# Kernel optimization log

Measured on AMD Instinct MI355X. Metric: run time of the kernel, lower is better.

The kernel has to match this reference:

```python
import jax, jax.numpy as jnp
import numpy as np

N = 50000
E = 800000
DIN = 64
DOUT = 64
H = 4
C = DOUT // H
EPS = 1e-5


def setup_inputs() -> dict:
    key = jax.random.key(0)
    ks = jax.random.split(key, 40)
    inp = {}
    inp["x"] = jax.random.normal(ks[0], (N, DIN), jnp.float32)
    inp["edge_index"] = jax.random.randint(ks[1], (2, E), 0, N, dtype=jnp.int32)
    inp["edge_weight"] = jax.random.uniform(ks[2], (E,), jnp.float32)
    inp["edge_attr"] = jax.random.normal(ks[3], (E, 1), jnp.float32)
    k = 4
    for i in range(2):
        din = DIN if i == 0 else DOUT
        s = din ** -0.5
        inp[f"gcn_w{i}"] = jax.random.normal(ks[k], (din, DOUT), jnp.float32) * s; k += 1
        inp[f"gcn_b{i}"] = jnp.zeros((DOUT,), jnp.float32)
        inp[f"res_w{i}"] = jax.random.normal(ks[k], (din, DOUT), jnp.float32) * s; k += 1
        inp[f"res_b{i}"] = jnp.zeros((DOUT,), jnp.float32)
        inp[f"ln_g{i}"] = jnp.ones((DOUT,), jnp.float32)
        inp[f"ln_b{i}"] = jnp.zeros((DOUT,), jnp.float32)
        sg = DOUT ** -0.5
        inp[f"gat_w{i}"] = jax.random.normal(ks[k], (DOUT, H * C), jnp.float32) * sg; k += 1
        inp[f"gat_b{i}"] = jnp.zeros((H * C,), jnp.float32)
        inp[f"att_src{i}"] = jax.random.normal(ks[k], (H, C), jnp.float32) * (C ** -0.5); k += 1
        inp[f"att_dst{i}"] = jax.random.normal(ks[k], (H, C), jnp.float32) * (C ** -0.5); k += 1
        inp[f"att_e{i}"] = jax.random.normal(ks[k], (H, C), jnp.float32) * (C ** -0.5); k += 1
        inp[f"ew_w{i}"] = jax.random.normal(ks[k], (1, H * C), jnp.float32); k += 1
    return inp


def _gcn(x, src0, dst0, ew, W, b):
    n = x.shape[0]
    sl = jnp.arange(n, dtype=src0.dtype)
    src = jnp.concatenate([src0, sl])
    dst = jnp.concatenate([dst0, sl])
    w = jnp.concatenate([ew, jnp.ones((n,), ew.dtype)])  # self-loop weight 1
    deg = jax.ops.segment_sum(w, dst, num_segments=n)
    dinv = jnp.where(deg > 0, jax.lax.rsqrt(deg), 0.0)
    norm = dinv[src] * w * dinv[dst]
    h = x @ W  # [n, DOUT]
    out = jax.ops.segment_sum(h[src] * norm[:, None], dst, num_segments=n)
    return out + b


def _gat(x, src0, dst0, ea, W, b, a_src, a_dst, a_e, We):
    n = x.shape[0]
    sl = jnp.arange(n, dtype=src0.dtype)
    src = jnp.concatenate([src0, sl])
    dst = jnp.concatenate([dst0, sl])
    loop_attr = jnp.broadcast_to(ea.mean(axis=0, keepdims=True), (n, ea.shape[1]))
    ea2 = jnp.concatenate([ea, loop_attr], axis=0)  # fill_value='mean'
    xl = (x @ W).reshape(n, H, C)
    a_s = (xl * a_src).sum(-1)  # [n,H]
    a_d = (xl * a_dst).sum(-1)
    a_ee = ((ea2 @ We).reshape(-1, H, C) * a_e).sum(-1)  # [E2,H]
    alpha = jax.nn.leaky_relu(a_s[src] + a_d[dst] + a_ee, 0.2)
    m = jax.ops.segment_max(alpha, dst, num_segments=n)
    e = jnp.exp(alpha - m[dst])
    s = jax.ops.segment_sum(e, dst, num_segments=n)
    alpha = e / (s[dst] + 1e-16)
    out = jax.ops.segment_sum(xl[src] * alpha[:, :, None], dst, num_segments=n)
    return out.reshape(n, H * C) + b


def _ln(x, g, b):
    mu = x.mean(-1, keepdims=True)
    v = ((x - mu) ** 2).mean(-1, keepdims=True)
    return (x - mu) * jax.lax.rsqrt(v + EPS) * g + b


def reference(x, edge_index, edge_weight, edge_attr,
              gcn_w0, gcn_b0, res_w0, res_b0, ln_g0, ln_b0,
              gat_w0, gat_b0, att_src0, att_dst0, att_e0, ew_w0,
              gcn_w1, gcn_b1, res_w1, res_b1, ln_g1, ln_b1,
              gat_w1, gat_b1, att_src1, att_dst1, att_e1, ew_w1):
    src0, dst0 = edge_index[0], edge_index[1]
    layers = [
        (gcn_w0, gcn_b0, res_w0, res_b0, ln_g0, ln_b0, gat_w0, gat_b0, att_src0, att_dst0, att_e0, ew_w0),
        (gcn_w1, gcn_b1, res_w1, res_b1, ln_g1, ln_b1, gat_w1, gat_b1, att_src1, att_dst1, att_e1, ew_w1),
    ]
    for (gw, gb, rw, rb, lg, lb, Wg, bg, a_s, a_d, a_e, We) in layers:
        residual = x @ rw + rb
        x = jax.nn.silu(_gcn(x, src0, dst0, edge_weight, gw, gb)) + residual
        x = _ln(x, lg, lb)
        x = jax.nn.silu(_gat(x, src0, dst0, edge_attr, Wg, bg, a_s, a_d, a_e, We)) + x
    return x  # down_sample=False -> Identity
```

## Files before the change

kernel.cpp:

```cpp
#include <hip/hip_runtime.h>
#include <hip/hip_fp16.h>

#define NN 50000
#define NE 800000
#define D 64
#define EPS 1e-5f
#define NT 3125
#define NB1 250
#define EPB 3200
#define NBIN 196
#define STOT 49152
#define SBLK 192

typedef unsigned short ushort_t;
typedef unsigned int uint_t;
typedef __attribute__((ext_vector_type(8))) short bf16x8;
typedef __attribute__((ext_vector_type(4))) float f32x4;

__device__ __forceinline__ float wave_sum64(float v) {
#pragma unroll
  for (int m = 1; m <= 32; m <<= 1) v += __shfl_xor(v, m, 64);
  return v;
}
__device__ __forceinline__ int wave_sum64i(int v) {
#pragma unroll
  for (int m = 1; m <= 32; m <<= 1) v += __shfl_xor(v, m, 64);
  return v;
}
__device__ __forceinline__ float group_sum16(float v) {
#pragma unroll
  for (int m = 1; m <= 8; m <<= 1) v += __shfl_xor(v, m, 64);
  return v;
}
__device__ __forceinline__ float silu_f(float v) { return v / (1.f + __expf(-v)); }
__device__ __forceinline__ float lrelu_f(float v) { return v >= 0.f ? v : 0.2f * v; }
__device__ __forceinline__ ushort_t f2b(float x) {
  unsigned u = __float_as_uint(x);
  return (ushort_t)((u + 0x7FFFu + ((u >> 16) & 1u)) >> 16);
}
__device__ __forceinline__ float b2f(ushort_t u) {
  return __uint_as_float(((unsigned)u) << 16);
}
__device__ __forceinline__ ushort_t f2h(float x) {
  return __half_as_ushort(__float2half_rn(x));
}
__device__ __forceinline__ float h2f(unsigned u) {
  return __half2float(__ushort_as_half((ushort_t)(u & 0xFFFFu)));
}
__device__ __forceinline__ float sel4(float a, float b, float c, float d, int h) {
  float ab = (h & 1) ? b : a;
  float cd = (h & 1) ? d : c;
  return (h & 2) ? cd : ab;
}
__device__ __forceinline__ bf16x8 pack8(float4 a, float4 b) {
  bf16x8 r;
  r[0] = (short)f2b(a.x); r[1] = (short)f2b(a.y);
  r[2] = (short)f2b(a.z); r[3] = (short)f2b(a.w);
  r[4] = (short)f2b(b.x); r[5] = (short)f2b(b.y);
  r[6] = (short)f2b(b.z); r[7] = (short)f2b(b.w);
  return r;
}

__global__ void __launch_bounds__(256) k_pre(
    const int* __restrict__ ei, int* __restrict__ histG,
    const float* __restrict__ x, const float* __restrict__ W1,
    const float* __restrict__ W2, const float* __restrict__ b2,
    ushort_t* __restrict__ out1, float* __restrict__ out2) {
  __shared__ __align__(16) char smem[16384];
  if (blockIdx.x < NB1) {
    int* h = (int*)smem;
    int blk = blockIdx.x;
    for (int j = threadIdx.x; j < NBIN; j += 256) h[j] = 0;
    __syncthreads();
    int e0 = blk * EPB;
    for (int e = e0 + threadIdx.x; e < e0 + EPB; e += 256)
      atomicAdd(&h[ei[NE + e] >> 8], 1);
    __syncthreads();
    for (int j = threadIdx.x; j < NBIN; j += 256) histG[j * NB1 + blk] = h[j];
    return;
  }
  ushort_t* wf = (ushort_t*)smem;
  for (int e = threadIdx.x; e < 8192; e += 256) {
    int f = e >> 9, r = e & 511;
    int lane = r >> 3, j = r & 7;
    int m = f >> 3, s = (f >> 2) & 1, t = f & 3;
    int k = s * 32 + (lane >> 4) * 8 + j;
    int n = t * 16 + (lane & 15);
    const float* Wm = m ? W2 : W1;
    wf[e] = f2b(Wm[k * D + n]);
  }
  __syncthreads();
  int tile = (blockIdx.x - NB1) * 4 + (threadIdx.x >> 6);
  if (tile >= NT) return;
  int l = threadIdx.x & 63;
  int q = l >> 4, cn = l & 15;
  const float* xr = x + ((size_t)tile * 16 + cn) * D + q * 8;
  float4 xa = *(const float4*)xr;
  float4 xb = *(const float4*)(xr + 4);
  float4 xc = *(const float4*)(xr + 32);
  float4 xd = *(const float4*)(xr + 36);
  bf16x8 a0 = pack8(xa, xb), a1 = pack8(xc, xd);
  f32x4 acc1[4], acc2[4];
#pragma unroll
  for (int t = 0; t < 4; ++t) {
    bf16x8 b10 = *(const bf16x8*)&wf[(0 * 8 + 0 * 4 + t) * 512 + l * 8];
    bf16x8 b11 = *(const bf16x8*)&wf[(0 * 8 + 1 * 4 + t) * 512 + l * 8];
    bf16x8 b20 = *(const bf16x8*)&wf[(1 * 8 + 0 * 4 + t) * 512 + l * 8];
    bf16x8 b21 = *(const bf16x8*)&wf[(1 * 8 + 1 * 4 + t) * 512 + l * 8];
    f32x4 z = {0.f, 0.f, 0.f, 0.f};
    acc1[t] = __builtin_amdgcn_mfma_f32_16x16x32_bf16(a0, b10, z, 0, 0, 0);
    acc1[t] = __builtin_amdgcn_mfma_f32_16x16x32_bf16(a1, b11, acc1[t], 0, 0, 0);
    acc2[t] = __builtin_amdgcn_mfma_f32_16x16x32_bf16(a0, b20, z, 0, 0, 0);
    acc2[t] = __builtin_amdgcn_mfma_f32_16x16x32_bf16(a1, b21, acc2[t], 0, 0, 0);
  }
#pragma unroll
  for (int t = 0; t < 4; ++t) {
    float bb = b2[t * 16 + cn];
#pragma unroll
    for (int r = 0; r < 4; ++r) {
      size_t row = (size_t)tile * 16 + q * 4 + r;
      out1[row * D + t * 16 + cn] = f2b(acc1[t][r]);
      out2[row * D + t * 16 + cn] = acc2[t][r] + bb;
    }
  }
}

__global__ void __launch_bounds__(256) k_scanA(
    int* __restrict__ histG, int* __restrict__ bsum, float* __restrict__ scal,
    const float* __restrict__ Wg0, const float* __restrict__ Wg1,
    const float* __restrict__ W11, const float* __restrict__ W21,
    const float* __restrict__ We0, const float* __restrict__ ae0,
    const float* __restrict__ We1, const float* __restrict__ ae1,
    ushort_t* __restrict__ wg16, ushort_t* __restrict__ wd16,
    float* __restrict__ wea2) {
  if (blockIdx.x == SBLK) {
    int tid = threadIdx.x;
    for (int t = tid; t < 1024; t += 256) scal[t] = 0.f;
    for (int e = tid; e < 4096; e += 256) {
      int f = e >> 9, r = e & 511;
      int lane = r >> 3, j = r & 7;
      int s = (f >> 2) & 1, t = f & 3;
      int k = s * 32 + (lane >> 4) * 8 + j;
      int n = t * 16 + (lane & 15);
      wg16[e] = f2b(Wg0[k * D + n]);
      wg16[4096 + e] = f2b(Wg1[k * D + n]);
    }
    for (int e = tid; e < 8192; e += 256) {
      int f = e >> 9, r = e & 511;
      int lane = r >> 3, j = r & 7;
      int m = f >> 3, s = (f >> 2) & 1, t = f & 3;
      int k = s * 32 + (lane >> 4) * 8 + j;
      int n = t * 16 + (lane & 15);
      const float* Wm = m ? W21 : W11;
      wd16[e] = f2b(Wm[k * D + n]);
    }
    if (tid < 64) {
      float v = group_sum16(We0[tid] * ae0[tid]);
      if ((tid & 15) == 0) wea2[tid >> 4] = v;
    } else if (tid < 128) {
      int c = tid - 64;
      float v = group_sum16(We1[c] * ae1[c]);
      if ((c & 15) == 0) wea2[4 + (c >> 4)] = v;
    }
    return;
  }
  __shared__ int sm[256];
  int j = threadIdx.x;
  int i = blockIdx.x * 256 + j;
  const int TOT = NBIN * NB1;
  int v = (i < TOT) ? histG[i] : 0;
  sm[j] = v;
  __syncthreads();
  for (int off = 1; off < 256; off <<= 1) {
    int t = (j >= off) ? sm[j - off] : 0;
    __syncthreads();
    sm[j] += t;
    __syncthreads();
  }
  if (i < TOT) histG[i] = sm[j] - v;
  if (j == 255) bsum[blockIdx.x] = sm[255];
}

__global__ void __launch_bounds__(256) k_scanC(int* __restrict__ histG,
                                               const int* __restrict__ bsum) {
  __shared__ int ws4[4];
  int t = threadIdx.x;
  int v = (t < (int)blockIdx.x) ? bsum[t] : 0;
  v = wave_sum64i(v);
  if ((t & 63) == 0) ws4[t >> 6] = v;
  __syncthreads();
  int prefix = ws4[0] + ws4[1] + ws4[2] + ws4[3];
  int i = blockIdx.x * 256 + t;
  if (i < NBIN * NB1) histG[i] += prefix;
}

__global__ void __launch_bounds__(256) k_part(
    const int* __restrict__ ei, const float* __restrict__ ew,
    const float* __restrict__ ea, const int* __restrict__ histG,
    uint2* __restrict__ rectmp, float* __restrict__ scal) {
  __shared__ int cur[NBIN];
  int blk = blockIdx.x;
  for (int j = threadIdx.x; j < NBIN; j += 256) cur[j] = histG[j * NB1 + blk];
  __syncthreads();
  int e0 = blk * EPB;
  float asum = 0.f;
  for (int e = e0 + threadIdx.x; e < e0 + EPB; e += 256) {
    int src = ei[e];
    int dst = ei[NE + e];
    float w = ew[e];
    float a = ea[e];
    asum += a;
    int slot = atomicAdd(&cur[dst >> 8], 1);
    uint2 r;
    r.x = (uint_t)(src & 0xFFFF) | ((uint_t)f2h(w) << 16);
    r.y = (uint_t)(dst & 0xFF) | ((uint_t)f2h(a) << 16);
    rectmp[slot] = r;
  }
  float s = wave_sum64(asum);
  if ((threadIdx.x & 63) == 0) {
    int slot = (blk * 4 + (threadIdx.x >> 6)) & 63;
    atomicAdd(&scal[(size_t)slot * 16], s);
  }
}

__global__ void __launch_bounds__(256) k_sfin(
    const uint2* __restrict__ rectmp, const int* __restrict__ histG,
    uint_t* __restrict__ recw, uint_t* __restrict__ reca, int* __restrict__ rs,
    float* __restrict__ dinv, float* __restrict__ scal) {
  __shared__ int cnt[256], sc[256], cur[256];
  __shared__ float wsum[256];
  int b = blockIdx.x;
  int t = threadIdx.x;
  int lo = histG[b * NB1];
  int hi = (b == NBIN - 1) ? NE : histG[(b + 1) * NB1];
  cnt[t] = 0;
  wsum[t] = 0.f;
  __syncthreads();
  for (int e = lo + t; e < hi; e += 256)
    atomicAdd(&cnt[rectmp[e].y & 0xFFu], 1);
  __syncthreads();
  int v = cnt[t];
  sc[t] = v;
  __syncthreads();
  for (int off = 1; off < 256; off <<= 1) {
    int u = (t >= off) ? sc[t - off] : 0;
    __syncthreads();
    sc[t] += u;
    __syncthreads();
  }
  int ex = sc[t] - v;
  int node = b * 256 + t;
  if (node < NN) rs[node] = lo + ex;
  if (b == NBIN - 1 && t == 0) rs[NN] = NE;
  cur[t] = lo + ex;
  __syncthreads();
  for (int e = lo + t; e < hi; e += 256) {
    uint2 r = rectmp[e];
    int dl = (int)(r.y & 0xFFu);
    int slot = atomicAdd(&cur[dl], 1);
    atomicAdd(&wsum[dl], h2f(r.x >> 16));
    uint_t src = r.x & 0xFFFFu;
    recw[slot] = r.x;
    reca[slot] = src | (r.y & 0xFFFF0000u);
  }
  __syncthreads();
  if (node < NN) dinv[node] = rsqrtf(1.f + wsum[t]);
  if (b == 0 && t == 0) {
    float s = 0.f;
    for (int j = 0; j < 64; ++j) s += scal[(size_t)j * 16];
    scal[1] = s / (float)NE;
  }
}

__global__ void __launch_bounds__(256) k_gcn_gat(
    const ushort_t* __restrict__ h16, const float* __restrict__ res,
    const float* __restrict__ dinv, const int* __restrict__ rs,
    const uint_t* __restrict__ recw,
    const float* __restrict__ gb, const float* __restrict__ lg,
    const float* __restrict__ lb,
    const ushort_t* __restrict__ wg, const float* __restrict__ att_src,
    const float* __restrict__ att_dst,
    float* __restrict__ x2, ushort_t* __restrict__ xl,
    float* __restrict__ a_s, float* __restrict__ a_d) {
  __shared__ int ss[4][64];
  __shared__ float swt[4][64];
  __shared__ __align__(16) ushort_t xt[16][72];
  int w = threadIdx.x >> 6;
  int l = threadIdx.x & 63;
  int base = blockIdx.x * 8;
  int iA = base + 2 * w;
  int iB = iA + 1;
  int half = l >> 5, cp = l & 31;
  float diA = dinv[iA], diB = dinv[iB];
  float accA = diA * diA * b2f(h16[(size_t)iA * D + l]);
  float accB = diB * diB * b2f(h16[(size_t)iB * D + l]);
  int kA = rs[iA], kA1 = rs[iA + 1];
  int kB = rs[iB], kB1 = rs[iB + 1];
  while (kA < kA1 || kB < kB1) {
    int cntA = min(32, kA1 - kA);
    int cntB = min(32, kB1 - kB);
    int src = 0; float wn = 0.f;
    if (half == 0) {
      if (cp < cntA) {
        uint_t r = recw[(size_t)(kA + cp)];
        src = (int)(r & 0xFFFFu);
        wn = dinv[src] * h2f(r >> 16) * diA;
      }
    } else {
      if (cp < cntB) {
        uint_t r = recw[(size_t)(kB + cp)];
        src = (int)(r & 0xFFFFu);
        wn = dinv[src] * h2f(r >> 16) * diB;
      }
    }
    ss[w][l] = src;
    swt[w][l] = wn;
    int nm = max(cntA, cntB);
    int j = 0;
    for (; j + 4 <= nm; j += 4) {
      int4 sa = *(const int4*)&ss[w][j];
      int4 sb = *(const int4*)&ss[w][32 + j];
      float4 wa = *(const float4*)&swt[w][j];
      float4 wb = *(const float4*)&swt[w][32 + j];
      float a0 = b2f(h16[(size_t)sa.x * D + l]);
      float b0 = b2f(h16[(size_t)sb.x * D + l]);
      float a1 = b2f(h16[(size_t)sa.y * D + l]);
      float b1 = b2f(h16[(size_t)sb.y * D + l]);
      float a2 = b2f(h16[(size_t)sa.z * D + l]);
      float b2v = b2f(h16[(size_t)sb.z * D + l]);
      float a3 = b2f(h16[(size_t)sa.w * D + l]);
      float b3 = b2f(h16[(size_t)sb.w * D + l]);
      accA = fmaf(wa.x, a0, accA); accB = fmaf(wb.x, b0, accB);
      accA = fmaf(wa.y, a1, accA); accB = fmaf(wb.y, b1, accB);
      accA = fmaf(wa.z, a2, accA); accB = fmaf(wb.z, b2v, accB);
      accA = fmaf(wa.w, a3, accA); accB = fmaf(wb.w, b3, accB);
    }
    for (; j < nm; ++j) {
      int sA = ss[w][j], sB = ss[w][32 + j];
      float wA = swt[w][j], wB = swt[w][32 + j];
      float vA = b2f(h16[(size_t)sA * D + l]);
      float vB = b2f(h16[(size_t)sB * D + l]);
      accA = fmaf(wA, vA, accA);
      accB = fmaf(wB, vB, accB);
    }
    kA += cntA; kB += cntB;
  }
  float gbv = gb[l], lgv = lg[l], lbv = lb[l];
  float x1A = silu_f(accA + gbv) + res[(size_t)iA * D + l];
  float x1B = silu_f(accB + gbv) + res[(size_t)iB * D + l];
  float muA = wave_sum64(x1A) * (1.f / 64.f);
  float muB = wave_sum64(x1B) * (1.f / 64.f);
  float dA = x1A - muA, dB = x1B - muB;
  float varA = wave_sum64(dA * dA) * (1.f / 64.f);
  float varB = wave_sum64(dB * dB) * (1.f / 64.f);
  float oA = dA * rsqrtf(varA + EPS) * lgv + lbv;
  float oB = dB * rsqrtf(varB + EPS) * lgv + lbv;
  x2[(size_t)iA * D + l] = oA;
  x2[(size_t)iB * D + l] = oB;
  xt[2 * w][l] = f2b(oA);
  xt[2 * w + 1][l] = f2b(oB);
  {
    ushort_t* xz = &xt[8][0];
    for (int e = threadIdx.x; e < 8 * 72; e += 256) xz[e] = 0;
  }
  __syncthreads();
  int t = w;
  int q = l >> 4, cn = l & 15;
  bf16x8 a0 = *(const bf16x8*)&xt[cn][q * 8];
  bf16x8 a1 = *(const bf16x8*)&xt[cn][q * 8 + 32];
  bf16x8 b0 = *(const bf16x8*)&wg[(size_t)((0 * 4 + t) * 512 + l * 8)];
  bf16x8 b1 = *(const bf16x8*)&wg[(size_t)((1 * 4 + t) * 512 + l * 8)];
  f32x4 z = {0.f, 0.f, 0.f, 0.f};
  f32x4 acc = __builtin_amdgcn_mfma_f32_16x16x32_bf16(a0, b0, z, 0, 0, 0);
  acc = __builtin_amdgcn_mfma_f32_16x16x32_bf16(a1, b1, acc, 0, 0, 0);
  if (q < 2) {
    float av = att_src[t * 16 + cn];
    float dv = att_dst[t * 16 + cn];
#pragma unroll
    for (int r = 0; r < 4; ++r) {
      size_t row = (size_t)base + q * 4 + r;
      xl[row * D + t * 16 + cn] = f2b(acc[r]);
      float vs = group_sum16(acc[r] * av);
      float vd = group_sum16(acc[r] * dv);
      if (cn == 0) {
        a_s[row * 4 + t] = vs;
        a_d[row * 4 + t] = vd;
      }
    }
  }
}

template <int FUSE>
__global__ void __launch_bounds__(256) k_gat_fin(
    const ushort_t* __restrict__ xl16, const float* __restrict__ x2,
    const float* __restrict__ a_s, const float* __restrict__ a_d,
    const int* __restrict__ rs, const uint_t* __restrict__ reca,
    const float* __restrict__ wea, const float* __restrict__ scal,
    const float* __restrict__ bg,
    const ushort_t* __restrict__ wd, const float* __restrict__ b2,
    ushort_t* __restrict__ out1, float* __restrict__ out2,
    float* __restrict__ xout) {
  __shared__ int ss[4][64];
  __shared__ float el[4][4][68];
  __shared__ __align__(16) ushort_t xt[16][72];
  int w = threadIdx.x >> 6;
  int base = blockIdx.x * 8;
  int iA = base + 2 * w;
  int iB = iA + 1;
  int l = threadIdx.x & 63;
  int half = l >> 5, cp = l & 31;
  int hh = l >> 4;
  float4 wv4 = *(const float4*)wea;
  float mean_attr = scal[1];
  float we_h = sel4(wv4.x, wv4.y, wv4.z, wv4.w, hh);
  float ad_hA = a_d[(size_t)iA * 4 + hh], as_iA = a_s[(size_t)iA * 4 + hh];
  float ad_hB = a_d[(size_t)iB * 4 + hh], as_iB = a_s[(size_t)iB * 4 + hh];
  float eSA = __expf(lrelu_f(as_iA + ad_hA + mean_attr * we_h));
  float eSB = __expf(lrelu_f(as_iB + ad_hB + mean_attr * we_h));
  float sA = eSA, sB = eSB;
  float accA = eSA * b2f(xl16[(size_t)iA * D + l]);
  float accB = eSB * b2f(xl16[(size_t)iB * D + l]);
  const float* adp = a_d + (size_t)(half ? iB : iA) * 4;
  float4 ad4 = *(const float4*)adp;
  int kA = rs[iA], kA1 = rs[iA + 1];
  int kB = rs[iB], kB1 = rs[iB + 1];
  while (kA < kA1 || kB < kB1) {
    int cntA = min(32, kA1 - kA);
    int cntB = min(32, kB1 - kB);
    int myk = half ? kB : kA;
    int mycnt = half ? cntB : cntA;
    int src = 0;
    float e0v = 0.f, e1v = 0.f, e2v = 0.f, e3v = 0.f;
    if (cp < mycnt) {
      uint_t r = reca[(size_t)(myk + cp)];
      src = (int)(r & 0xFFFFu);
      float ea = h2f(r >> 16);
      float4 as4 = *(const float4*)(a_s + (size_t)src * 4);
      e0v = __expf(lrelu_f(as4.x + fmaf(ea, wv4.x, ad4.x)));
      e1v = __expf(lrelu_f(as4.y + fmaf(ea, wv4.y, ad4.y)));
      e2v = __expf(lrelu_f(as4.z + fmaf(ea, wv4.z, ad4.z)));
      e3v = __expf(lrelu_f(as4.w + fmaf(ea, wv4.w, ad4.w)));
    }
    ss[w][l] = src;
    el[w][0][l] = e0v;
    el[w][1][l] = e1v;
    el[w][2][l] = e2v;
    el[w][3][l] = e3v;
    int nm = max(cntA, cntB);
    int j = 0;
    for (; j + 4 <= nm; j += 4) {
      int4 sa = *(const int4*)&ss[w][j];
      int4 sb = *(const int4*)&ss[w][32 + j];
      float4 ea4 = *(const float4*)&el[w][hh][j];
      float4 eb4 = *(const float4*)&el[w][hh][32 + j];
      float a0 = b2f(xl16[(size_t)sa.x * D + l]);
      float b0 = b2f(xl16[(size_t)sb.x * D + l]);
      float a1 = b2f(xl16[(size_t)sa.y * D + l]);
      float b1 = b2f(xl16[(size_t)sb.y * D + l]);
      float a2 = b2f(xl16[(size_t)sa.z * D + l]);
      float b2v = b2f(xl16[(size_t)sb.z * D + l]);
      float a3 = b2f(xl16[(size_t)sa.w * D + l]);
      float b3 = b2f(xl16[(size_t)sb.w * D + l]);
      accA = fmaf(ea4.x, a0, accA); accB = fmaf(eb4.x, b0, accB);
      accA = fmaf(ea4.y, a1, accA); accB = fmaf(eb4.y, b1, accB);
      accA = fmaf(ea4.z, a2, accA); accB = fmaf(eb4.z, b2v, accB);
      accA = fmaf(ea4.w, a3, accA); accB = fmaf(eb4.w, b3, accB);
      sA += (ea4.x + ea4.y) + (ea4.z + ea4.w);
      sB += (eb4.x + eb4.y) + (eb4.z + eb4.w);
    }
    for (; j < nm; ++j) {
      int srcA = ss[w][j], srcB = ss[w][32 + j];
      float eA = el[w][hh][j], eB = el[w][hh][32 + j];
      float vA = b2f(xl16[(size_t)srcA * D + l]);
      float vB = b2f(xl16[(size_t)srcB * D + l]);
      accA = fmaf(eA, vA, accA);
      accB = fmaf(eB, vB, accB);
      sA += eA; sB += eB;
    }
    kA += cntA; kB += cntB;
  }
  float bgv = bg[l];
  float oA = accA / (sA + 1e-16f) + bgv;
  float oB = accB / (sB + 1e-16f) + bgv;
  float vA = silu_f(oA) + x2[(size_t)iA * D + l];
  float vB = silu_f(oB) + x2[(size_t)iB * D + l];
  if (FUSE) {
    xt[2 * w][l] = f2b(vA);
    xt[2 * w + 1][l] = f2b(vB);
    {
      ushort_t* xz = &xt[8][0];
      for (int e = threadIdx.x; e < 8 * 72; e += 256) xz[e] = 0;
    }
    __syncthreads();
    int t = w;
    int q = l >> 4, cn = l & 15;
    bf16x8 a0 = *(const bf16x8*)&xt[cn][q * 8];
    bf16x8 a1 = *(const bf16x8*)&xt[cn][q * 8 + 32];
#pragma unroll
    for (int m = 0; m < 2; ++m) {
      bf16x8 b0 = *(const bf16x8*)&wd[(size_t)((m * 8 + 0 * 4 + t) * 512 + l * 8)];
      bf16x8 b1 = *(const bf16x8*)&wd[(size_t)((m * 8 + 1 * 4 + t) * 512 + l * 8)];
      f32x4 z = {0.f, 0.f, 0.f, 0.f};
      f32x4 acc = __builtin_amdgcn_mfma_f32_16x16x32_bf16(a0, b0, z, 0, 0, 0);
      acc = __builtin_amdgcn_mfma_f32_16x16x32_bf16(a1, b1, acc, 0, 0, 0);
      if (q < 2) {
        float bb = (m == 1) ? b2[t * 16 + cn] : 0.f;
#pragma unroll
        for (int r = 0; r < 4; ++r) {
          size_t row = (size_t)base + q * 4 + r;
          if (m == 0)
            out1[row * D + t * 16 + cn] = f2b(acc[r]);
          else
            out2[row * D + t * 16 + cn] = acc[r] + bb;
        }
      }
    }
  } else {
    xout[(size_t)iA * D + l] = vA;
    xout[(size_t)iB * D + l] = vB;
  }
}


extern "C" void kernel_launch(void* const* d_in, const int* in_sizes, int n_in,
                              void* d_out, int out_size, void* d_ws, size_t ws_size,
                              hipStream_t stream) {
  (void)in_sizes; (void)n_in; (void)out_size; (void)ws_size;
  const float* x  = (const float*)d_in[0];
  const int*   ei = (const int*)d_in[1];
  const float* ew = (const float*)d_in[2];
  const float* ea = (const float*)d_in[3];
  const float* P[2][12];
  for (int l = 0; l < 2; ++l)
    for (int j = 0; j < 12; ++j) P[l][j] = (const float*)d_in[4 + l * 12 + j];

  float* W = (float*)d_ws;
  const size_t o_rs    = 0;
  const size_t o_dinv  = o_rs + NN + 16;
  const size_t o_wea   = o_dinv + NN;
  const size_t o_scal  = o_wea + 16;
  const size_t o_bsum  = o_scal + 1024;
  const size_t o_hist  = o_bsum + 256;
  const size_t o_recw  = o_hist + STOT;
  const size_t o_reca  = o_recw + NE;
  const size_t o_rtmp  = o_reca + NE;
  const size_t o_h16   = o_rtmp + (size_t)NE * 2;
  const size_t o_xl16  = o_h16 + (size_t)NN * D / 2;
  const size_t o_res   = o_xl16 + (size_t)NN * D / 2;
  const size_t o_x2    = o_res + (size_t)NN * D;
  const size_t o_as    = o_x2 + (size_t)NN * D;
  const size_t o_ad    = o_as + (size_t)NN * 4;
  const size_t o_wg16  = o_ad + (size_t)NN * 4;
  const size_t o_wd16  = o_wg16 + 4096;

  int*      rs    = (int*)(W + o_rs);
  float*    dinv  = W + o_dinv;
  float*    wea2  = W + o_wea;
  float*    scal  = W + o_scal;
  int*      bsum  = (int*)(W + o_bsum);
  int*      histG = (int*)(W + o_hist);
  uint_t*   recw  = (uint_t*)(W + o_recw);
  uint_t*   reca  = (uint_t*)(W + o_reca);
  uint2*    rtmp  = (uint2*)(W + o_rtmp);
  ushort_t* h16   = (ushort_t*)(W + o_h16);
  ushort_t* xl16  = (ushort_t*)(W + o_xl16);
  float*    resb  = W + o_res;
  float*    x2b   = W + o_x2;
  float*    asb   = W + o_as;
  float*    adb   = W + o_ad;
  ushort_t* wg16  = (ushort_t*)(W + o_wg16);
  ushort_t* wd16  = (ushort_t*)(W + o_wd16);

  const int B = 256;
  const int gPre = NB1 + (NT + 3) / 4;
  const int gN2  = NN / 8;

  k_pre<<<gPre, B, 0, stream>>>(ei, histG, x, P[0][0], P[0][2], P[0][3], h16, resb);
  k_scanA<<<SBLK + 1, B, 0, stream>>>(histG, bsum, scal,
                                      P[0][6], P[1][6], P[1][0], P[1][2],
                                      P[0][11], P[0][10], P[1][11], P[1][10],
                                      wg16, wd16, wea2);
  k_scanC<<<SBLK, B, 0, stream>>>(histG, bsum);
  k_part<<<NB1, B, 0, stream>>>(ei, ew, ea, histG, rtmp, scal);
  k_sfin<<<NBIN, B, 0, stream>>>(rtmp, histG, recw, reca, rs, dinv, scal);

  k_gcn_gat<<<gN2, B, 0, stream>>>(h16, resb, dinv, rs, recw,
                                   P[0][1], P[0][4], P[0][5],
                                   wg16, P[0][8], P[0][9],
                                   x2b, xl16, asb, adb);
  k_gat_fin<1><<<gN2, B, 0, stream>>>(xl16, x2b, asb, adb, rs, reca,
                                      wea2, scal, P[0][7],
                                      wd16, P[1][3], h16, resb, nullptr);
  k_gcn_gat<<<gN2, B, 0, stream>>>(h16, resb, dinv, rs, recw,
                                   P[1][1], P[1][4], P[1][5],
                                   wg16 + 4096, P[1][8], P[1][9],
                                   x2b, xl16, asb, adb);
  k_gat_fin<0><<<gN2, B, 0, stream>>>(xl16, x2b, asb, adb, rs, reca,
                                      wea2 + 4, scal, P[1][7],
                                      nullptr, nullptr, nullptr, nullptr,
                                      (float*)d_out);
}
```

Baseline: 293.7 us.

## Remap gather lanes so each half-wave handles one node with 2 features per lane

In the GCN and GAT aggregation kernels, each wave used to process two nodes with every lane gathering one bf16 feature for both nodes. Now each 32-lane half-wave owns one node and each lane loads a packed 32-bit pair of bf16 features per neighbor. This halves the number of gather load instructions and issues wider loads, with per-node reductions done over 32 lanes. The cost is that the loop still runs to the max of the two nodes' degrees, so the half with fewer neighbors idles.

```diff
diff --git a/kernel.cpp b/kernel.cpp
--- a/kernel.cpp
+++ b/kernel.cpp
@@ -22,6 +22,11 @@
   for (int m = 1; m <= 32; m <<= 1) v += __shfl_xor(v, m, 64);
   return v;
 }
+__device__ __forceinline__ float half_sum32(float v) {
+#pragma unroll
+  for (int m = 1; m <= 16; m <<= 1) v += __shfl_xor(v, m, 64);
+  return v;
+}
 __device__ __forceinline__ int wave_sum64i(int v) {
 #pragma unroll
   for (int m = 1; m <= 32; m <<= 1) v += __shfl_xor(v, m, 64);
@@ -40,6 +45,12 @@
 }
 __device__ __forceinline__ float b2f(ushort_t u) {
   return __uint_as_float(((unsigned)u) << 16);
+}
+__device__ __forceinline__ float b2f_lo(uint_t u) {
+  return __uint_as_float(u << 16);
+}
+__device__ __forceinline__ float b2f_hi(uint_t u) {
+  return __uint_as_float(u & 0xFFFF0000u);
 }
 __device__ __forceinline__ ushort_t f2h(float x) {
   return __half_as_ushort(__float2half_rn(x));
@@ -288,77 +299,70 @@
   int w = threadIdx.x >> 6;
   int l = threadIdx.x & 63;
   int base = blockIdx.x * 8;
+  int half = l >> 5, c = l & 31;
   int iA = base + 2 * w;
   int iB = iA + 1;
-  int half = l >> 5, cp = l & 31;
-  float diA = dinv[iA], diB = dinv[iB];
-  float accA = diA * diA * b2f(h16[(size_t)iA * D + l]);
-  float accB = diB * diB * b2f(h16[(size_t)iB * D + l]);
+  int i = iA + half;
+  float di = dinv[i];
+  uint_t u0 = *(const uint_t*)&h16[(size_t)i * D + 2 * c];
+  float dii = di * di;
+  float acc0 = dii * b2f_lo(u0);
+  float acc1 = dii * b2f_hi(u0);
   int kA = rs[iA], kA1 = rs[iA + 1];
   int kB = rs[iB], kB1 = rs[iB + 1];
+  int sbase = half * 32;
   while (kA < kA1 || kB < kB1) {
     int cntA = min(32, kA1 - kA);
     int cntB = min(32, kB1 - kB);
+    int myk = half ? kB : kA;
+    int mycnt = half ? cntB : cntA;
     int src = 0; float wn = 0.f;
-    if (half == 0) {
-      if (cp < cntA) {
-        uint_t r = recw[(size_t)(kA + cp)];
-        src = (int)(r & 0xFFFFu);
-        wn = dinv[src] * h2f(r >> 16) * diA;
-      }
-    } else {
-      if (cp < cntB) {
-        uint_t r = recw[(size_t)(kB + cp)];
-        src = (int)(r & 0xFFFFu);
-        wn = dinv[src] * h2f(r >> 16) * diB;
-      }
+    if (c < mycnt) {
+      uint_t r = recw[(size_t)(myk + c)];
+      src = (int)(r & 0xFFFFu);
+      wn = dinv[src] * h2f(r >> 16) * di;
     }
     ss[w][l] = src;
     swt[w][l] = wn;
     int nm = max(cntA, cntB);
     int j = 0;
     for (; j + 4 <= nm; j += 4) {
-      int4 sa = *(const int4*)&ss[w][j];
-      int4 sb = *(const int4*)&ss[w][32 + j];
-      float4 wa = *(const float4*)&swt[w][j];
-      float4 wb = *(const float4*)&swt[w][32 + j];
-      float a0 = b2f(h16[(size_t)sa.x * D + l]);
-      float b0 = b2f(h16[(size_t)sb.x * D + l]);
-      float a1 = b2f(h16[(size_t)sa.y * D + l]);
-      float b1 = b2f(h16[(size_t)sb.y * D + l]);
-      float a2 = b2f(h16[(size_t)sa.z * D + l]);
-      float b2v = b2f(h16[(size_t)sb.z * D + l]);
-      float a3 = b2f(h16[(size_t)sa.w * D + l]);
-      float b3 = b2f(h16[(size_t)sb.w * D + l]);
-      accA = fmaf(wa.x, a0, accA); accB = fmaf(wb.x, b0, accB);
-      accA = fmaf(wa.y, a1, accA); accB = fmaf(wb.y, b1, accB);
-      accA = fmaf(wa.z, a2, accA); accB = fmaf(wb.z, b2v, accB);
-      accA = fmaf(wa.w, a3, accA); accB = fmaf(wb.w, b3, accB);
+      int4 s4 = *(const int4*)&ss[w][sbase + j];
+      float4 w4 = *(const float4*)&swt[w][sbase + j];
+      uint_t ua = *(const uint_t*)&h16[(size_t)s4.x * D + 2 * c];
+      uint_t ub = *(const uint_t*)&h16[(size_t)s4.y * D + 2 * c];
+      uint_t uc = *(const uint_t*)&h16[(size_t)s4.z * D + 2 * c];
+      uint_t ud = *(const uint_t*)&h16[(size_t)s4.w * D + 2 * c];
+      acc0 = fmaf(w4.x, b2f_lo(ua), acc0); acc1 = fmaf(w4.x, b2f_hi(ua), acc1);
+      acc0 = fmaf(w4.y, b2f_lo(ub), acc0); acc1 = fmaf(w4.y, b2f_hi(ub), acc1);
+      acc0 = fmaf(w4.z, b2f_lo(uc), acc0); acc1 = fmaf(w4.z, b2f_hi(uc), acc1);
+      acc0 = fmaf(w4.w, b2f_lo(ud), acc0); acc1 = fmaf(w4.w, b2f_hi(ud), acc1);
     }
     for (; j < nm; ++j) {
-      int sA = ss[w][j], sB = ss[w][32 + j];
-      float wA = swt[w][j], wB = swt[w][32 + j];
-      float vA = b2f(h16[(size_t)sA * D + l]);
-      float vB = b2f(h16[(size_t)sB * D + l]);
-      accA = fmaf(wA, vA, accA);
-      accB = fmaf(wB, vB, accB);
+      int s1 = ss[w][sbase + j];
+      float w1 = swt[w][sbase + j];
+      uint_t u = *(const uint_t*)&h16[(size_t)s1 * D + 2 * c];
+      acc0 = fmaf(w1, b2f_lo(u), acc0);
+      acc1 = fmaf(w1, b2f_hi(u), acc1);
     }
     kA += cntA; kB += cntB;
   }
-  float gbv = gb[l], lgv = lg[l], lbv = lb[l];
-  float x1A = silu_f(accA + gbv) + res[(size_t)iA * D + l];
-  float x1B = silu_f(accB + gbv) + res[(size_t)iB * D + l];
-  float muA = wave_sum64(x1A) * (1.f / 64.f);
-  float muB = wave_sum64(x1B) * (1.f / 64.f);
-  float dA = x1A - muA, dB = x1B - muB;
-  float varA = wave_sum64(dA * dA) * (1.f / 64.f);
-  float varB = wave_sum64(dB * dB) * (1.f / 64.f);
-  float oA = dA * rsqrtf(varA + EPS) * lgv + lbv;
-  float oB = dB * rsqrtf(varB + EPS) * lgv + lbv;
-  x2[(size_t)iA * D + l] = oA;
-  x2[(size_t)iB * D + l] = oB;
-  xt[2 * w][l] = f2b(oA);
-  xt[2 * w + 1][l] = f2b(oB);
+  float2 gb2 = *(const float2*)&gb[2 * c];
+  float2 lg2 = *(const float2*)&lg[2 * c];
+  float2 lb2 = *(const float2*)&lb[2 * c];
+  float2 rs2 = *(const float2*)&res[(size_t)i * D + 2 * c];
+  float x0 = silu_f(acc0 + gb2.x) + rs2.x;
+  float x1 = silu_f(acc1 + gb2.y) + rs2.y;
+  float mu = half_sum32(x0 + x1) * (1.f / 64.f);
+  float d0 = x0 - mu, d1 = x1 - mu;
+  float var = half_sum32(d0 * d0 + d1 * d1) * (1.f / 64.f);
+  float rinv = rsqrtf(var + EPS);
+  float o0 = d0 * rinv * lg2.x + lb2.x;
+  float o1 = d1 * rinv * lg2.y + lb2.y;
+  float2 o2; o2.x = o0; o2.y = o1;
+  *(float2*)&x2[(size_t)i * D + 2 * c] = o2;
+  uint_t pk = (uint_t)f2b(o0) | ((uint_t)f2b(o1) << 16);
+  *(uint_t*)&xt[2 * w + half][2 * c] = pk;
   {
     ushort_t* xz = &xt[8][0];
     for (int e = threadIdx.x; e < 8 * 72; e += 256) xz[e] = 0;
@@ -404,26 +408,27 @@
   __shared__ float el[4][4][68];
   __shared__ __align__(16) ushort_t xt[16][72];
   int w = threadIdx.x >> 6;
+  int l = threadIdx.x & 63;
   int base = blockIdx.x * 8;
+  int half = l >> 5, c = l & 31;
   int iA = base + 2 * w;
   int iB = iA + 1;
-  int l = threadIdx.x & 63;
-  int half = l >> 5, cp = l & 31;
-  int hh = l >> 4;
+  int i = iA + half;
+  int hh = c >> 3;
   float4 wv4 = *(const float4*)wea;
   float mean_attr = scal[1];
   float we_h = sel4(wv4.x, wv4.y, wv4.z, wv4.w, hh);
-  float ad_hA = a_d[(size_t)iA * 4 + hh], as_iA = a_s[(size_t)iA * 4 + hh];
-  float ad_hB = a_d[(size_t)iB * 4 + hh], as_iB = a_s[(size_t)iB * 4 + hh];
-  float eSA = __expf(lrelu_f(as_iA + ad_hA + mean_attr * we_h));
-  float eSB = __expf(lrelu_f(as_iB + ad_hB + mean_attr * we_h));
-  float sA = eSA, sB = eSB;
-  float accA = eSA * b2f(xl16[(size_t)iA * D + l]);
-  float accB = eSB * b2f(xl16[(size_t)iB * D + l]);
-  const float* adp = a_d + (size_t)(half ? iB : iA) * 4;
-  float4 ad4 = *(const float4*)adp;
+  float ad_h = a_d[(size_t)i * 4 + hh];
+  float as_i = a_s[(size_t)i * 4 + hh];
+  float eS = __expf(lrelu_f(as_i + ad_h + mean_attr * we_h));
+  float s = eS;
+  uint_t u0 = *(const uint_t*)&xl16[(size_t)i * D + 2 * c];
+  float acc0 = eS * b2f_lo(u0);
+  float acc1 = eS * b2f_hi(u0);
+  float4 ad4 = *(const float4*)(a_d + (size_t)i * 4);
   int kA = rs[iA], kA1 = rs[iA + 1];
   int kB = rs[iB], kB1 = rs[iB + 1];
+  int sbase = half * 32;
   while (kA < kA1 || kB < kB1) {
     int cntA = min(32, kA1 - kA);
     int cntB = min(32, kB1 - kB);
@@ -431,8 +436,8 @@
     int mycnt = half ? cntB : cntA;
     int src = 0;
     float e0v = 0.f, e1v = 0.f, e2v = 0.f, e3v = 0.f;
-    if (cp < mycnt) {
-      uint_t r = reca[(size_t)(myk + cp)];
+    if (c < mycnt) {
+      uint_t r = reca[(size_t)(myk + c)];
       src = (int)(r & 0xFFFFu);
       float ea = h2f(r >> 16);
       float4 as4 = *(const float4*)(a_s + (size_t)src * 4);
@@ -449,44 +454,38 @@
     int nm = max(cntA, cntB);
     int j = 0;
     for (; j + 4 <= nm; j += 4) {
-      int4 sa = *(const int4*)&ss[w][j];
-      int4 sb = *(const int4*)&ss[w][32 + j];
-      float4 ea4 = *(const float4*)&el[w][hh][j];
-      float4 eb4 = *(const float4*)&el[w][hh][32 + j];
-      float a0 = b2f(xl16[(size_t)sa.x * D + l]);
-      float b0 = b2f(xl16[(size_t)sb.x * D + l]);
-      float a1 = b2f(xl16[(size_t)sa.y * D + l]);
-      float b1 = b2f(xl16[(size_t)sb.y * D + l]);
-      float a2 = b2f(xl16[(size_t)sa.z * D + l]);
-      float b2v = b2f(xl16[(size_t)sb.z * D + l]);
-      float a3 = b2f(xl16[(size_t)sa.w * D + l]);
-      float b3 = b2f(xl16[(size_t)sb.w * D + l]);
-      accA = fmaf(ea4.x, a0, accA); accB = fmaf(eb4.x, b0, accB);
-      accA = fmaf(ea4.y, a1, accA); accB = fmaf(eb4.y, b1, accB);
-      accA = fmaf(ea4.z, a2, accA); accB = fmaf(eb4.z, b2v, accB);
-      accA = fmaf(ea4.w, a3, accA); accB = fmaf(eb4.w, b3, accB);
-      sA += (ea4.x + ea4.y) + (ea4.z + ea4.w);
-      sB += (eb4.x + eb4.y) + (eb4.z + eb4.w);
+      int4 s4 = *(const int4*)&ss[w][sbase + j];
+      float4 e4 = *(const float4*)&el[w][hh][sbase + j];
+      uint_t ua = *(const uint_t*)&xl16[(size_t)s4.x * D + 2 * c];
+      uint_t ub = *(const uint_t*)&xl16[(size_t)s4.y * D + 2 * c];
+      uint_t uc = *(const uint_t*)&xl16[(size_t)s4.z * D + 2 * c];
+      uint_t ud = *(const uint_t*)&xl16[(size_t)s4.w * D + 2 * c];
+      acc0 = fmaf(e4.x, b2f_lo(ua), acc0); acc1 = fmaf(e4.x, b2f_hi(ua), acc1);
+      acc0 = fmaf(e4.y, b2f_lo(ub), acc0); acc1 = fmaf(e4.y, b2f_hi(ub), acc1);
+      acc0 = fmaf(e4.z, b2f_lo(uc), acc0); acc1 = fmaf(e4.z, b2f_hi(uc), acc1);
+      acc0 = fmaf(e4.w, b2f_lo(ud), acc0); acc1 = fmaf(e4.w, b2f_hi(ud), acc1);
+      s += (e4.x + e4.y) + (e4.z + e4.w);
     }
     for (; j < nm; ++j) {
-      int srcA = ss[w][j], srcB = ss[w][32 + j];
-      float eA = el[w][hh][j], eB = el[w][hh][32 + j];
-      float vA = b2f(xl16[(size_t)srcA * D + l]);
-      float vB = b2f(xl16[(size_t)srcB * D + l]);
-      accA = fmaf(eA, vA, accA);
-      accB = fmaf(eB, vB, accB);
-      sA += eA; sB += eB;
+      int s1 = ss[w][sbase + j];
+      float e1 = el[w][hh][sbase + j];
+      uint_t u = *(const uint_t*)&xl16[(size_t)s1 * D + 2 * c];
+      acc0 = fmaf(e1, b2f_lo(u), acc0);
+      acc1 = fmaf(e1, b2f_hi(u), acc1);
+      s += e1;
     }
     kA += cntA; kB += cntB;
   }
-  float bgv = bg[l];
-  float oA = accA / (sA + 1e-16f) + bgv;
-  float oB = accB / (sB + 1e-16f) + bgv;
-  float vA = silu_f(oA) + x2[(size_t)iA * D + l];
-  float vB = silu_f(oB) + x2[(size_t)iB * D + l];
+  float2 bg2 = *(const float2*)&bg[2 * c];
+  float rcp = 1.f / (s + 1e-16f);
+  float o0 = acc0 * rcp + bg2.x;
+  float o1 = acc1 * rcp + bg2.y;
+  float2 x22 = *(const float2*)&x2[(size_t)i * D + 2 * c];
+  float v0 = silu_f(o0) + x22.x;
+  float v1 = silu_f(o1) + x22.y;
   if (FUSE) {
-    xt[2 * w][l] = f2b(vA);
-    xt[2 * w + 1][l] = f2b(vB);
+    uint_t pk = (uint_t)f2b(v0) | ((uint_t)f2b(v1) << 16);
+    *(uint_t*)&xt[2 * w + half][2 * c] = pk;
     {
       ushort_t* xz = &xt[8][0];
       for (int e = threadIdx.x; e < 8 * 72; e += 256) xz[e] = 0;
@@ -516,8 +515,8 @@
       }
     }
   } else {
-    xout[(size_t)iA * D + l] = vA;
-    xout[(size_t)iB * D + l] = vB;
+    float2 v2; v2.x = v0; v2.y = v1;
+    *(float2*)&xout[(size_t)i * D + 2 * c] = v2;
   }
 }
 
```

Result: faster. 285.5 us (-2.8%).
